# Kernel tuning notes

Hardware: AMD Instinct MI355X
Metric: run time of the kernel (lower is better)

## Reference

```python
import jax, jax.numpy as jnp
import numpy as np

NUM_WIRES = 4
NUM_LAYERS = 2
BATCH = 1_048_576


def _rz(theta):
    # diag(e^{-i t/2}, e^{+i t/2})
    e = jnp.exp(-0.5j * theta.astype(jnp.complex64))
    z = jnp.zeros((), jnp.complex64)
    return jnp.stack([jnp.stack([e, z]), jnp.stack([z, jnp.conj(e)])])


def _rx(theta):
    c = jnp.cos(0.5 * theta).astype(jnp.complex64)
    s = (-1j * jnp.sin(0.5 * theta)).astype(jnp.complex64)
    return jnp.stack([jnp.stack([c, s]), jnp.stack([s, c])])


def _apply_1q(state, U, w):
    # state: (B,2,2,2,2); apply 2x2 unitary U on wire w (axis w+1)
    s = jnp.moveaxis(state, w + 1, -1)
    s = jnp.einsum('...i,ji->...j', s, U)
    return jnp.moveaxis(s, -1, w + 1)


def _cnot(state, c, t):
    # flip target axis where control bit == 1
    s = jnp.moveaxis(state, (c + 1, t + 1), (-2, -1))
    s = jnp.stack([s[..., 0, :], s[..., 1, ::-1]], axis=-2)
    return jnp.moveaxis(s, (-2, -1), (c + 1, t + 1))


def _circuit(x, params):
    # RY(x_i)|0> per wire gives product state [cos(x_i/2), sin(x_i/2)]
    h = 0.5 * x
    a = jnp.stack([jnp.cos(h), jnp.sin(h)], axis=-1).astype(jnp.complex64)  # (B,4,2)
    state = jnp.einsum('bi,bj,bk,bl->bijkl', a[:, 0], a[:, 1], a[:, 2], a[:, 3])
    for layer in range(NUM_LAYERS):
        for w in range(NUM_WIRES):
            # RZ then RX on wire w, fused into one 2x2 unitary
            U = _rx(params[layer, w, 1]) @ _rz(params[layer, w, 0])
            state = _apply_1q(state, U, w)
        for w in range(NUM_WIRES - 1):
            state = _cnot(state, w, w + 1)
        state = _cnot(state, NUM_WIRES - 1, 0)
    probs = state.real ** 2 + state.imag ** 2  # (B,2,2,2,2)
    evs = []
    for w in range(NUM_WIRES):
        axes = tuple(ax for ax in range(1, NUM_WIRES + 1) if ax != w + 1)
        p = jnp.sum(probs, axis=axes)  # (B,2) marginal of wire w
        evs.append(p[:, 0] - p[:, 1])  # <Z_w>
    return jnp.stack(evs, axis=-1)  # (B,4)


def setup_inputs() -> dict:
    key = jax.random.key(0)
    k1, k2 = jax.random.split(key)
    x = jax.random.normal(k1, (BATCH, NUM_WIRES), dtype=jnp.float32)
    params = jax.random.normal(k2, (NUM_LAYERS, NUM_WIRES, 2), dtype=jnp.float32)
    return {"x": x, "params": params}


def reference(x, params):
    return _circuit(x, params)
```

## Files before the change

### kernel.cpp

```cpp
#include <hip/hip_runtime.h>

#define NUM_WIRES 4
#define NUM_LAYERS 2


#define INV_4PI 0.07957747154594767f

__global__ void gate_prep(const float* __restrict__ params, float* __restrict__ g) {
    const int t = threadIdx.x;
    if (t < 4) {
        const float p0 = params[t * 2 + 0];
        const float p1 = params[t * 2 + 1];
        float cz, sz, cx, sx;
        __sincosf(0.5f * p0, &sz, &cz);
        __sincosf(0.5f * p1, &sx, &cx);
        g[t * 4 + 0] = cx * cz;
        g[t * 4 + 1] = cx * sz;
        g[t * 4 + 2] = sx * sz;
        g[t * 4 + 3] = sx * cz;
    } else if (t < 8) {
        const int w = t - 4;
        const float p1 = params[(NUM_WIRES + w) * 2 + 1];
        float cx, sx;
        __sincosf(0.5f * p1, &sx, &cx);
        g[16 + w * 2] = cx;
        g[17 + w * 2] = sx;
    } else if (t >= 16 && t < 32) {
        const int i = t - 16;
        float dr = 1.f, di = 0.f;
        for (int w = 0; w < NUM_WIRES; ++w) {
            const float p0 = params[(NUM_WIRES + w) * 2 + 0];
            float c, s;
            __sincosf(0.5f * p0, &s, &c);
            const float sg = ((i >> (3 - w)) & 1) ? s : -s;
            const float ndr = dr * c - di * sg;
            const float ndi = dr * sg + di * c;
            dr = ndr; di = ndi;
        }
        g[24 + i * 2] = dr;
        g[25 + i * 2] = di;
    }
}

__device__ __forceinline__ float rfl(float v) {
    return __int_as_float(__builtin_amdgcn_readfirstlane(__float_as_int(v)));
}

__device__ __forceinline__ void cmul(float ar, float ai, float br, float bi,
                                     float& orr, float& oi) {
    orr = fmaf(ar, br, -(ai * bi));
    oi  = fmaf(ar, bi,   ai * br);
}

template <int CM, int TM>
__device__ __forceinline__ void cnot(float zr[16], float zi[16]) {
#pragma unroll
    for (int i = 0; i < 16; ++i) {
        if ((i & CM) && !(i & TM)) {
            const int j = i | TM;
            float t;
            t = zr[i]; zr[i] = zr[j]; zr[j] = t;
            t = zi[i]; zi[i] = zi[j]; zi[j] = t;
        }
    }
}

__global__ __launch_bounds__(256) void qsim_kernel(const float* __restrict__ x,
                                                   const float* __restrict__ gf,
                                                   float* __restrict__ out, int batch) {
    const int b = blockIdx.x * 256 + threadIdx.x;
    if (b >= batch) return;

    float G[56];
#pragma unroll
    for (int k = 0; k < 14; ++k) {
        const float4 v = reinterpret_cast<const float4*>(gf)[k];
        G[4 * k + 0] = rfl(v.x);
        G[4 * k + 1] = rfl(v.y);
        G[4 * k + 2] = rfl(v.z);
        G[4 * k + 3] = rfl(v.w);
    }

    const float4 xv = reinterpret_cast<const float4*>(x)[b];

    float fr[4][2], fi[4][2];
    {
        const float xs[4] = {xv.x, xv.y, xv.z, xv.w};
#pragma unroll
        for (int w = 0; w < 4; ++w) {
            const float r = xs[w] * INV_4PI;
            const float s = __builtin_amdgcn_sinf(r);
            const float c = __builtin_amdgcn_cosf(r);
            const float A = G[w * 4 + 0], B = G[w * 4 + 1];
            const float C = G[w * 4 + 2], D = G[w * 4 + 3];
            fr[w][0] = fmaf(A, c, C * s);
            fi[w][0] = fmaf(-B, c, -(D * s));
            fr[w][1] = fmaf(A, s, -(C * c));
            fi[w][1] = fmaf(B, s, -(D * c));
        }
    }

    float mr[4], mi[4], nr[4], ni[4];
#pragma unroll
    for (int p = 0; p < 2; ++p)
#pragma unroll
        for (int q = 0; q < 2; ++q) {
            cmul(fr[0][p], fi[0][p], fr[1][q], fi[1][q], mr[p * 2 + q], mi[p * 2 + q]);
            cmul(fr[2][p], fi[2][p], fr[3][q], fi[3][q], nr[p * 2 + q], ni[p * 2 + q]);
        }
    float zr[16], zi[16];
#pragma unroll
    for (int i = 0; i < 16; ++i)
        cmul(mr[i >> 2], mi[i >> 2], nr[i & 3], ni[i & 3], zr[i], zi[i]);

    cnot<8, 4>(zr, zi);
    cnot<4, 2>(zr, zi);
    cnot<2, 1>(zr, zi);
    cnot<1, 8>(zr, zi);

#pragma unroll
    for (int i = 0; i < 16; ++i) {
        const float dr = G[24 + i * 2], di = G[25 + i * 2];
        const float ar = zr[i], ai = zi[i];
        zr[i] = fmaf(dr, ar, -(di * ai));
        zi[i] = fmaf(dr, ai,   di * ar);
    }

#pragma unroll
    for (int w = 0; w < 4; ++w) {
        const float c = G[16 + w * 2], s = G[17 + w * 2];
        const int M = 8 >> w;
#pragma unroll
        for (int i = 0; i < 16; ++i) {
            if (!(i & M)) {
                const int j = i | M;
                const float ar = zr[i], ai = zi[i];
                const float br = zr[j], bi = zi[j];
                zr[i] = fmaf(c, ar,   s * bi);
                zi[i] = fmaf(c, ai, -(s * br));
                zr[j] = fmaf(c, br,   s * ai);
                zi[j] = fmaf(c, bi, -(s * ar));
            }
        }
    }

    cnot<8, 4>(zr, zi);
    cnot<4, 2>(zr, zi);
    cnot<2, 1>(zr, zi);
    cnot<1, 8>(zr, zi);

    float p[16];
#pragma unroll
    for (int i = 0; i < 16; ++i) p[i] = fmaf(zr[i], zr[i], zi[i] * zi[i]);

    float d0[8], s1[8];
#pragma unroll
    for (int k = 0; k < 8; ++k) {
        d0[k] = p[2 * k] - p[2 * k + 1];
        s1[k] = p[2 * k] + p[2 * k + 1];
    }
    const float e3 = ((d0[0] + d0[1]) + (d0[2] + d0[3])) + ((d0[4] + d0[5]) + (d0[6] + d0[7]));
    const float e2 = ((s1[0] - s1[1]) + (s1[2] - s1[3])) + ((s1[4] - s1[5]) + (s1[6] - s1[7]));
    float s2[4];
#pragma unroll
    for (int k = 0; k < 4; ++k) s2[k] = s1[2 * k] + s1[2 * k + 1];
    const float e1 = (s2[0] - s2[1]) + (s2[2] - s2[3]);
    const float e0 = (s2[0] + s2[1]) - (s2[2] + s2[3]);

    reinterpret_cast<float4*>(out)[b] = make_float4(e0, e1, e2, e3);
}

extern "C" void kernel_launch(void* const* d_in, const int* in_sizes, int n_in,
                              void* d_out, int out_size, void* d_ws, size_t ws_size,
                              hipStream_t stream) {
    const float* x = (const float*)d_in[0];
    const float* params = (const float*)d_in[1];
    float* out = (float*)d_out;
    float* g = (float*)d_ws;
    const int batch = in_sizes[0] / NUM_WIRES;

    gate_prep<<<1, 64, 0, stream>>>(params, g);
    const int blocks = (batch + 255) / 256;
    qsim_kernel<<<blocks, 256, 0, stream>>>(x, g, out, batch);
}
```

Baseline: 77.96 us.

## Process two batch elements per thread using packed float2 FMA math

Each thread now simulates two circuits, with the state held in 2-wide float vectors so the compiler can emit packed FP32 instructions (v_pk_fma_f32 and related). The grid shrinks by half and the per-thread gate-constant loads are amortised over two samples. In exchange, register pressure roughly doubles, which may lower occupancy, and the sin/cos calls remain scalar.

```diff
diff --git a/kernel.cpp b/kernel.cpp
--- a/kernel.cpp
+++ b/kernel.cpp
@@ -5,6 +5,8 @@
 
 
 #define INV_4PI 0.07957747154594767f
+
+typedef float v2 __attribute__((ext_vector_type(2)));
 
 __global__ void gate_prep(const float* __restrict__ params, float* __restrict__ g) {
     const int t = threadIdx.x;
@@ -46,19 +48,21 @@
     return __int_as_float(__builtin_amdgcn_readfirstlane(__float_as_int(v)));
 }
 
-__device__ __forceinline__ void cmul(float ar, float ai, float br, float bi,
-                                     float& orr, float& oi) {
-    orr = fmaf(ar, br, -(ai * bi));
-    oi  = fmaf(ar, bi,   ai * br);
+__device__ __forceinline__ v2 ef(v2 a, v2 b, v2 c) { return __builtin_elementwise_fma(a, b, c); }
+__device__ __forceinline__ v2 sp(float x) { v2 r; r.x = x; r.y = x; return r; }
+
+__device__ __forceinline__ void cmul(v2 ar, v2 ai, v2 br, v2 bi, v2& orr, v2& oi) {
+    orr = ef(ar, br, -(ai * bi));
+    oi  = ef(ar, bi,   ai * br);
 }
 
 template <int CM, int TM>
-__device__ __forceinline__ void cnot(float zr[16], float zi[16]) {
+__device__ __forceinline__ void cnot(v2 zr[16], v2 zi[16]) {
 #pragma unroll
     for (int i = 0; i < 16; ++i) {
         if ((i & CM) && !(i & TM)) {
             const int j = i | TM;
-            float t;
+            v2 t;
             t = zr[i]; zr[i] = zr[j]; zr[j] = t;
             t = zi[i]; zi[i] = zi[j]; zi[j] = t;
         }
@@ -68,8 +72,9 @@
 __global__ __launch_bounds__(256) void qsim_kernel(const float* __restrict__ x,
                                                    const float* __restrict__ gf,
                                                    float* __restrict__ out, int batch) {
-    const int b = blockIdx.x * 256 + threadIdx.x;
-    if (b >= batch) return;
+    const int tid = threadIdx.x;
+    const int i0 = blockIdx.x * 512 + tid;
+    const int i1 = i0 + 256;
 
     float G[56];
 #pragma unroll
@@ -81,26 +86,35 @@
         G[4 * k + 3] = rfl(v.w);
     }
 
-    const float4 xv = reinterpret_cast<const float4*>(x)[b];
-
-    float fr[4][2], fi[4][2];
-    {
-        const float xs[4] = {xv.x, xv.y, xv.z, xv.w};
-#pragma unroll
-        for (int w = 0; w < 4; ++w) {
-            const float r = xs[w] * INV_4PI;
-            const float s = __builtin_amdgcn_sinf(r);
-            const float c = __builtin_amdgcn_cosf(r);
-            const float A = G[w * 4 + 0], B = G[w * 4 + 1];
-            const float C = G[w * 4 + 2], D = G[w * 4 + 3];
-            fr[w][0] = fmaf(A, c, C * s);
-            fi[w][0] = fmaf(-B, c, -(D * s));
-            fr[w][1] = fmaf(A, s, -(C * c));
-            fi[w][1] = fmaf(B, s, -(D * c));
-        }
-    }
-
-    float mr[4], mi[4], nr[4], ni[4];
+    const float4 xa = (i0 < batch) ? reinterpret_cast<const float4*>(x)[i0]
+                                   : make_float4(0.f, 0.f, 0.f, 0.f);
+    const float4 xb = (i1 < batch) ? reinterpret_cast<const float4*>(x)[i1]
+                                   : make_float4(0.f, 0.f, 0.f, 0.f);
+
+    v2 xs[4];
+    xs[0].x = xa.x; xs[0].y = xb.x;
+    xs[1].x = xa.y; xs[1].y = xb.y;
+    xs[2].x = xa.z; xs[2].y = xb.z;
+    xs[3].x = xa.w; xs[3].y = xb.w;
+
+    v2 fr[4][2], fi[4][2];
+#pragma unroll
+    for (int w = 0; w < 4; ++w) {
+        const v2 r = xs[w] * sp(INV_4PI);
+        v2 s, c;
+        s.x = __builtin_amdgcn_sinf(r.x);
+        s.y = __builtin_amdgcn_sinf(r.y);
+        c.x = __builtin_amdgcn_cosf(r.x);
+        c.y = __builtin_amdgcn_cosf(r.y);
+        const float A = G[w * 4 + 0], B = G[w * 4 + 1];
+        const float C = G[w * 4 + 2], D = G[w * 4 + 3];
+        fr[w][0] = ef(sp(A), c, sp(C) * s);
+        fi[w][0] = ef(sp(-B), c, -(sp(D) * s));
+        fr[w][1] = ef(sp(A), s, -(sp(C) * c));
+        fi[w][1] = ef(sp(B), s, -(sp(D) * c));
+    }
+
+    v2 mr[4], mi[4], nr[4], ni[4];
 #pragma unroll
     for (int p = 0; p < 2; ++p)
 #pragma unroll
@@ -108,7 +122,7 @@
             cmul(fr[0][p], fi[0][p], fr[1][q], fi[1][q], mr[p * 2 + q], mi[p * 2 + q]);
             cmul(fr[2][p], fi[2][p], fr[3][q], fi[3][q], nr[p * 2 + q], ni[p * 2 + q]);
         }
-    float zr[16], zi[16];
+    v2 zr[16], zi[16];
 #pragma unroll
     for (int i = 0; i < 16; ++i)
         cmul(mr[i >> 2], mi[i >> 2], nr[i & 3], ni[i & 3], zr[i], zi[i]);
@@ -121,25 +135,25 @@
 #pragma unroll
     for (int i = 0; i < 16; ++i) {
         const float dr = G[24 + i * 2], di = G[25 + i * 2];
-        const float ar = zr[i], ai = zi[i];
-        zr[i] = fmaf(dr, ar, -(di * ai));
-        zi[i] = fmaf(dr, ai,   di * ar);
+        const v2 ar = zr[i], ai = zi[i];
+        zr[i] = ef(sp(dr), ar, -(sp(di) * ai));
+        zi[i] = ef(sp(dr), ai,   sp(di) * ar);
     }
 
 #pragma unroll
     for (int w = 0; w < 4; ++w) {
-        const float c = G[16 + w * 2], s = G[17 + w * 2];
+        const v2 c = sp(G[16 + w * 2]), s = sp(G[17 + w * 2]);
         const int M = 8 >> w;
 #pragma unroll
         for (int i = 0; i < 16; ++i) {
             if (!(i & M)) {
                 const int j = i | M;
-                const float ar = zr[i], ai = zi[i];
-                const float br = zr[j], bi = zi[j];
-                zr[i] = fmaf(c, ar,   s * bi);
-                zi[i] = fmaf(c, ai, -(s * br));
-                zr[j] = fmaf(c, br,   s * ai);
-                zi[j] = fmaf(c, bi, -(s * ar));
+                const v2 ar = zr[i], ai = zi[i];
+                const v2 br = zr[j], bi = zi[j];
+                zr[i] = ef(c, ar,   s * bi);
+                zi[i] = ef(c, ai, -(s * br));
+                zr[j] = ef(c, br,   s * ai);
+                zi[j] = ef(c, bi, -(s * ar));
             }
         }
     }
@@ -149,25 +163,28 @@
     cnot<2, 1>(zr, zi);
     cnot<1, 8>(zr, zi);
 
-    float p[16];
-#pragma unroll
-    for (int i = 0; i < 16; ++i) p[i] = fmaf(zr[i], zr[i], zi[i] * zi[i]);
-
-    float d0[8], s1[8];
+    v2 p[16];
+#pragma unroll
+    for (int i = 0; i < 16; ++i) p[i] = ef(zr[i], zr[i], zi[i] * zi[i]);
+
+    v2 d0[8], s1[8];
 #pragma unroll
     for (int k = 0; k < 8; ++k) {
         d0[k] = p[2 * k] - p[2 * k + 1];
         s1[k] = p[2 * k] + p[2 * k + 1];
     }
-    const float e3 = ((d0[0] + d0[1]) + (d0[2] + d0[3])) + ((d0[4] + d0[5]) + (d0[6] + d0[7]));
-    const float e2 = ((s1[0] - s1[1]) + (s1[2] - s1[3])) + ((s1[4] - s1[5]) + (s1[6] - s1[7]));
-    float s2[4];
+    const v2 e3 = ((d0[0] + d0[1]) + (d0[2] + d0[3])) + ((d0[4] + d0[5]) + (d0[6] + d0[7]));
+    const v2 e2 = ((s1[0] - s1[1]) + (s1[2] - s1[3])) + ((s1[4] - s1[5]) + (s1[6] - s1[7]));
+    v2 s2[4];
 #pragma unroll
     for (int k = 0; k < 4; ++k) s2[k] = s1[2 * k] + s1[2 * k + 1];
-    const float e1 = (s2[0] - s2[1]) + (s2[2] - s2[3]);
-    const float e0 = (s2[0] + s2[1]) - (s2[2] + s2[3]);
-
-    reinterpret_cast<float4*>(out)[b] = make_float4(e0, e1, e2, e3);
+    const v2 e1 = (s2[0] - s2[1]) + (s2[2] - s2[3]);
+    const v2 e0 = (s2[0] + s2[1]) - (s2[2] + s2[3]);
+
+    if (i0 < batch)
+        reinterpret_cast<float4*>(out)[i0] = make_float4(e0.x, e1.x, e2.x, e3.x);
+    if (i1 < batch)
+        reinterpret_cast<float4*>(out)[i1] = make_float4(e0.y, e1.y, e2.y, e3.y);
 }
 
 extern "C" void kernel_launch(void* const* d_in, const int* in_sizes, int n_in,
@@ -180,6 +197,6 @@
     const int batch = in_sizes[0] / NUM_WIRES;
 
     gate_prep<<<1, 64, 0, stream>>>(params, g);
-    const int blocks = (batch + 255) / 256;
+    const int blocks = (batch + 511) / 512;
     qsim_kernel<<<blocks, 256, 0, stream>>>(x, g, out, batch);
 }
```

Result: slower. 80.15 us (+2.8%).
